# Optimization experiments

Measured on AMD Instinct MI355X. Metric: run time of the kernel, lower is better.

## Reference

```python
import jax, jax.numpy as jnp
import numpy as np

EPS_NORM = 1e-12   # F.normalize eps
EPS_Q = 1e-5       # quant scale clamp

def simple_rmsnorm(x):
    # F.normalize(x, dim=-1) * sqrt(dim)  ==  x / sqrt(mean(x^2))
    d = x.shape[-1]
    n = jnp.maximum(jnp.linalg.norm(x, axis=-1, keepdims=True), EPS_NORM)
    return x / n * jnp.sqrt(jnp.asarray(d, x.dtype))

def activation_quant(x):
    # per-token 8-bit absmax quant
    scale = 127.0 / jnp.clip(jnp.max(jnp.abs(x), axis=-1, keepdims=True), EPS_Q, None)
    return jnp.clip(jnp.round(x * scale), -128.0, 127.0) / scale

def weight_quant(w):
    # per-tensor ternary quant: scale = 1 / mean|w|
    scale = 1.0 / jnp.clip(jnp.mean(jnp.abs(w)), EPS_Q, None)
    return jnp.clip(jnp.round(w * scale), -1.0, 1.0) / scale

def bitlinear158(x, w):
    xn = simple_rmsnorm(x)
    # straight-through estimators
    xq = xn + jax.lax.stop_gradient(activation_quant(xn) - xn)
    wq = w + jax.lax.stop_gradient(weight_quant(w) - w)
    # w is [out, in] like nn.Linear
    return jnp.einsum('bsd,od->bso', xq, wq)

def setup_inputs() -> dict:
    key = jax.random.key(0)
    k1, k2, k3 = jax.random.split(key, 3)
    dim, inner = 2048, 8192
    x = jax.random.normal(k1, (4, 2048, dim), dtype=jnp.float32)
    w1 = jax.random.normal(k2, (inner, dim), dtype=jnp.float32) * 0.02
    w2 = jax.random.normal(k3, (dim, inner), dtype=jnp.float32) * 0.02
    return {"x": x, "w1": w1, "w2": w2}

def reference(x, w1, w2):
    h = bitlinear158(x, w1)
    h = jax.nn.gelu(h, approximate=False)  # nn.GELU() default = exact erf
    return bitlinear158(h, w2)
```

## Files before the change

### kernel.cpp

```cpp
#include <hip/hip_runtime.h>
#include <hip/hip_bf16.h>
#include <hip/hip_fp16.h>

typedef __attribute__((ext_vector_type(4))) int i32x4;
typedef __attribute__((ext_vector_type(8))) unsigned short u16x8;
typedef __attribute__((ext_vector_type(8))) char c8;
typedef __attribute__((ext_vector_type(4))) char c4;
typedef unsigned int u32;
typedef unsigned short u16;

#define SCH0() __builtin_amdgcn_sched_barrier(0)

__device__ __forceinline__ void gload_lds16(const void* g, void* l) {
  __builtin_amdgcn_global_load_lds((const u32 __attribute__((address_space(1)))*)g,
                                   (u32 __attribute__((address_space(3)))*)l, 16, 0, 0);
}
__device__ __forceinline__ float h2f(u16 u) { return __half2float(__ushort_as_half(u)); }
__device__ __forceinline__ u16  f2h(float f){ return __half_as_ushort(__float2half_rn(f)); }

__global__ __launch_bounds__(256) void quant_x_kernel(const float* __restrict__ x,
    char* __restrict__ qx, float* __restrict__ invs) {
  const int D = 2048;
  int row = blockIdx.x, tid = threadIdx.x;
  const float* xr = x + (size_t)row * D;
  float4 a = ((const float4*)xr)[tid * 2], b = ((const float4*)xr)[tid * 2 + 1];
  float v[8] = {a.x, a.y, a.z, a.w, b.x, b.y, b.z, b.w};
  double ss = 0; float mx = 0.0f;
#pragma unroll
  for (int i = 0; i < 8; i++) { ss += (double)v[i] * v[i]; mx = fmaxf(mx, fabsf(v[i])); }
  __shared__ double sd[256]; __shared__ float sf[256];
  sd[tid] = ss; sf[tid] = mx; __syncthreads();
  for (int o = 128; o > 0; o >>= 1) {
    if (tid < o) { sd[tid] += sd[tid + o]; sf[tid] = fmaxf(sf[tid], sf[tid + o]); }
    __syncthreads();
  }
  __shared__ float bn, bs;
  if (tid == 0) {
    float n = fmaxf((float)sqrt(sd[0]), 1e-12f);
    float amax = sf[0] * (sqrtf((float)D) / n);
    float cl = fmaxf(amax, 1e-5f);
    bn = n; bs = 127.0f / cl;
    invs[row] = cl / 127.0f;
  }
  __syncthreads();
  float n = bn, s = bs, sq = sqrtf((float)D);
  c8 q;
#pragma unroll
  for (int i = 0; i < 8; i++) {
    float xn = (v[i] / n) * sq;
    float r = rintf(xn * s);
    r = fminf(fmaxf(r, -128.0f), 127.0f);
    q[i] = (char)(int)r;
  }
  *(c8*)&qx[(size_t)row * D + tid * 8] = q;
}

__global__ __launch_bounds__(256) void absum_partial(const float* __restrict__ w,
    double* __restrict__ part, int n4) {
  int tid = threadIdx.x;
  double s = 0;
  for (int i = blockIdx.x * 256 + tid; i < n4; i += gridDim.x * 256) {
    float4 v = ((const float4*)w)[i];
    s += (double)fabsf(v.x) + (double)fabsf(v.y) + (double)fabsf(v.z) + (double)fabsf(v.w);
  }
  __shared__ double sd[256];
  sd[tid] = s; __syncthreads();
  for (int o = 128; o > 0; o >>= 1) { if (tid < o) sd[tid] += sd[tid + o]; __syncthreads(); }
  if (tid == 0) part[blockIdx.x] = sd[0];
}

__global__ __launch_bounds__(256) void wscale_final(const double* __restrict__ part,
    float* __restrict__ wsc) {
  int tid = threadIdx.x;
  __shared__ double sd[256];
  sd[tid] = part[tid] + part[tid + 256]; __syncthreads();
  for (int o = 128; o > 0; o >>= 1) { if (tid < o) sd[tid] += sd[tid + o]; __syncthreads(); }
  double s1 = sd[0]; __syncthreads();
  sd[tid] = part[512 + tid] + part[768 + tid]; __syncthreads();
  for (int o = 128; o > 0; o >>= 1) { if (tid < o) sd[tid] += sd[tid + o]; __syncthreads(); }
  if (tid == 0) {
    float m1 = (float)(s1 / 16777216.0);
    float m2 = (float)(sd[0] / 16777216.0);
    float d1 = fmaxf(m1, 1e-5f), d2 = fmaxf(m2, 1e-5f);
    wsc[0] = 1.0f / d1; wsc[1] = d1; wsc[2] = 1.0f / d2; wsc[3] = d2;
  }
}

__global__ __launch_bounds__(256) void quant_w_kernel(const float* __restrict__ w,
    char* __restrict__ q, const float* __restrict__ wsc, int widx, int n4) {
  float s = wsc[widx];
  for (int i = blockIdx.x * 256 + threadIdx.x; i < n4; i += gridDim.x * 256) {
    float4 v = ((const float4*)w)[i];
    c4 o;
    o[0] = (char)(int)(fminf(fmaxf(rintf(v.x * s), -1.0f), 1.0f));
    o[1] = (char)(int)(fminf(fmaxf(rintf(v.y * s), -1.0f), 1.0f));
    o[2] = (char)(int)(fminf(fmaxf(rintf(v.z * s), -1.0f), 1.0f));
    o[3] = (char)(int)(fminf(fmaxf(rintf(v.w * s), -1.0f), 1.0f));
    ((c4*)q)[i] = o;
  }
}

template <int EPI>
__global__ __launch_bounds__(256, 4) void gemm128(const char* __restrict__ A,
    const char* __restrict__ B, int N, int K, size_t ldA, size_t ldB, int gridN,
    const float* __restrict__ rowscale, const float* __restrict__ wsc,
    int widx, void* __restrict__ outp) {
  __shared__ __align__(16) char sm[2][2][8192];
  const int tid = threadIdx.x;
  const int lane = tid & 63, w = tid >> 6;
  const int wm = w >> 1, wn = w & 1;
  const int llo = lane & 15, lhi = lane >> 4;
  const int koff = ((lhi ^ ((llo >> 1) & 3)) << 4);

  const int nwg = gridDim.x, cpx = nwg >> 3;
  const int swz = (blockIdx.x & 7) * cpx + (blockIdx.x >> 3);
  const int bm = swz / gridN, bn = swz % gridN;

  const int NT = K >> 6;
  const size_t Abase = (size_t)(bm * 128) * ldA;
  const size_t Bbase = (size_t)(bn * 128) * ldB;

  const int r0 = tid >> 2;
  const int kb0 = (((tid & 3) ^ ((tid >> 3) & 3)) << 4);

  auto stage_tile = [&](int buf, int kt) {
    size_t ko = (size_t)kt * 64;
    gload_lds16(A + Abase + (size_t)r0 * ldA + ko + kb0,        &sm[buf][0][tid * 16]);
    gload_lds16(A + Abase + (size_t)(64 + r0) * ldA + ko + kb0, &sm[buf][0][4096 + tid * 16]);
    gload_lds16(B + Bbase + (size_t)r0 * ldB + ko + kb0,        &sm[buf][1][tid * 16]);
    gload_lds16(B + Bbase + (size_t)(64 + r0) * ldB + ko + kb0, &sm[buf][1][4096 + tid * 16]);
  };

  i32x4 a[4], b[4];
  auto readAB = [&](int buf) {
    int ra = wm * 64 + llo, rb = wn * 64 + llo;
#pragma unroll
    for (int f = 0; f < 4; f++)
      a[f] = *(const i32x4*)&sm[buf][0][(ra + f * 16) * 64 + koff];
#pragma unroll
    for (int f = 0; f < 4; f++)
      b[f] = *(const i32x4*)&sm[buf][1][(rb + f * 16) * 64 + koff];
  };

  i32x4 acc[4][4];
#pragma unroll
  for (int m = 0; m < 4; m++)
#pragma unroll
    for (int n = 0; n < 4; n++) acc[m][n] = (i32x4){0, 0, 0, 0};

  stage_tile(0, 0);
  asm volatile("s_nop 0" ::: "memory");
  stage_tile(1, 1);
  asm volatile("s_waitcnt vmcnt(4)\n\ts_barrier" ::: "memory");

  for (int t = 0; t < NT; t++) {
    const int cur = t & 1;
    readAB(cur);
    asm volatile("s_waitcnt lgkmcnt(0)\n\ts_barrier" ::: "memory");
    if (t + 2 < NT) stage_tile(cur, t + 2);
    SCH0();
    __builtin_amdgcn_s_setprio(1);
#pragma unroll
    for (int m = 0; m < 4; m++)
#pragma unroll
      for (int n = 0; n < 4; n++)
        acc[m][n] = __builtin_amdgcn_mfma_i32_16x16x64_i8(a[m], b[n], acc[m][n], 0, 0, 0);
    __builtin_amdgcn_s_setprio(0);
    if (t + 1 < NT) {
      if (t + 2 < NT) asm volatile("s_waitcnt vmcnt(4)\n\ts_barrier" ::: "memory");
      else            asm volatile("s_waitcnt vmcnt(0)\n\ts_barrier" ::: "memory");
    }
  }

  float wdeq = wsc[widx];
#pragma unroll
  for (int mf = 0; mf < 4; mf++) {
#pragma unroll
    for (int reg = 0; reg < 4; reg++) {
      int r = bm * 128 + wm * 64 + mf * 16 + lhi * 4 + reg;
      float deq = rowscale[r] * wdeq;
#pragma unroll
      for (int nf = 0; nf < 4; nf++) {
        int c = bn * 128 + wn * 64 + nf * 16 + llo;
        float val = (float)acc[mf][nf][reg] * deq;
        if (EPI == 0) {
          float g = 0.5f * val * (1.0f + erff(val * 0.70710678118654752440f));
          ((u16*)outp)[(size_t)r * N + c] = f2h(g);
        } else {
          ((float*)outp)[(size_t)r * N + c] = val;
        }
      }
    }
  }
}

__global__ __launch_bounds__(256) void quant_h_kernel(u16* __restrict__ h, float* __restrict__ invs) {
  const int D = 8192;
  int row = blockIdx.x, tid = threadIdx.x;
  u16* hr = h + (size_t)row * D;
  float v[32];
#pragma unroll
  for (int j = 0; j < 4; j++) {
    u16x8 u = *(const u16x8*)&hr[j * 2048 + tid * 8];
#pragma unroll
    for (int e = 0; e < 8; e++) v[j * 8 + e] = h2f(u[e]);
  }
  double ss = 0; float mx = 0.0f;
#pragma unroll
  for (int i = 0; i < 32; i++) { ss += (double)v[i] * v[i]; mx = fmaxf(mx, fabsf(v[i])); }
  __shared__ double sd[256]; __shared__ float sf[256];
  sd[tid] = ss; sf[tid] = mx; __syncthreads();
  for (int o = 128; o > 0; o >>= 1) {
    if (tid < o) { sd[tid] += sd[tid + o]; sf[tid] = fmaxf(sf[tid], sf[tid + o]); }
    __syncthreads();
  }
  __shared__ float bn, bs;
  if (tid == 0) {
    float n = fmaxf((float)sqrt(sd[0]), 1e-12f);
    float amax = sf[0] * (sqrtf((float)D) / n);
    float cl = fmaxf(amax, 1e-5f);
    bn = n; bs = 127.0f / cl;
    invs[row] = cl / 127.0f;
  }
  __syncthreads();
  float n = bn, s = bs, sq = sqrtf((float)D);
  char* hq = (char*)hr;
#pragma unroll
  for (int j = 0; j < 4; j++) {
    c8 q;
#pragma unroll
    for (int e = 0; e < 8; e++) {
      float xn = (v[j * 8 + e] / n) * sq;
      float r = rintf(xn * s);
      r = fminf(fmaxf(r, -128.0f), 127.0f);
      q[e] = (char)(int)r;
    }
    *(c8*)&hq[j * 2048 + tid * 8] = q;
  }
}

extern "C" void kernel_launch(void* const* d_in, const int* in_sizes, int n_in,
                              void* d_out, int out_size, void* d_ws, size_t ws_size,
                              hipStream_t stream) {
  const float* x  = (const float*)d_in[0];
  const float* w1 = (const float*)d_in[1];
  const float* w2 = (const float*)d_in[2];

  char* ws = (char*)d_ws;
  char*   qx     = (char*)(ws + 0);
  char*   w1q    = (char*)(ws + 16777216);
  char*   w2q    = (char*)(ws + 33554432);
  u16*    h      = (u16*)(ws + 50331648);
  float*  invs_x = (float*)(ws + 184549376);
  float*  invs_h = (float*)(ws + 184582144);
  double* part   = (double*)(ws + 184614912);
  float*  wsc    = (float*)(ws + 184623104);

  quant_x_kernel<<<8192, 256, 0, stream>>>(x, qx, invs_x);
  absum_partial<<<512, 256, 0, stream>>>(w1, part, 4194304);
  absum_partial<<<512, 256, 0, stream>>>(w2, part + 512, 4194304);
  wscale_final<<<1, 256, 0, stream>>>(part, wsc);
  quant_w_kernel<<<2048, 256, 0, stream>>>(w1, w1q, wsc, 0, 4194304);
  quant_w_kernel<<<2048, 256, 0, stream>>>(w2, w2q, wsc, 2, 4194304);
  gemm128<0><<<4096, 256, 0, stream>>>(qx, w1q, 8192, 2048, 2048, 2048, 64,
                                       invs_x, wsc, 1, (void*)h);
  quant_h_kernel<<<8192, 256, 0, stream>>>(h, invs_h);
  gemm128<1><<<1024, 256, 0, stream>>>((const char*)h, w2q, 2048, 8192, 16384, 8192, 16,
                                       invs_h, wsc, 3, d_out);
}
```

Before: 489.4 us.

## Load GEMM fragments directly from global memory, dropping LDS staging

Replaces the LDS double-buffered global_load_lds pipeline in the int8 GEMM with per-wave direct global loads of MFMA fragments into registers. This removes barriers, LDS traffic and the staging bookkeeping. In exchange it loses data sharing between waves (each A/B row tile is fetched by two waves) and the explicit prefetch overlap, relying on the L2/L1 caches and compiler scheduling instead.

```diff
diff --git a/kernel.cpp b/kernel.cpp
--- a/kernel.cpp
+++ b/kernel.cpp
@@ -9,12 +9,6 @@
 typedef unsigned int u32;
 typedef unsigned short u16;
 
-#define SCH0() __builtin_amdgcn_sched_barrier(0)
-
-__device__ __forceinline__ void gload_lds16(const void* g, void* l) {
-  __builtin_amdgcn_global_load_lds((const u32 __attribute__((address_space(1)))*)g,
-                                   (u32 __attribute__((address_space(3)))*)l, 16, 0, 0);
-}
 __device__ __forceinline__ float h2f(u16 u) { return __half2float(__ushort_as_half(u)); }
 __device__ __forceinline__ u16  f2h(float f){ return __half_as_ushort(__float2half_rn(f)); }
 
@@ -101,46 +95,28 @@
 }
 
 template <int EPI>
-__global__ __launch_bounds__(256, 4) void gemm128(const char* __restrict__ A,
+__global__ __launch_bounds__(256, 4) void gemm_dr(const char* __restrict__ A,
     const char* __restrict__ B, int N, int K, size_t ldA, size_t ldB, int gridN,
     const float* __restrict__ rowscale, const float* __restrict__ wsc,
     int widx, void* __restrict__ outp) {
-  __shared__ __align__(16) char sm[2][2][8192];
   const int tid = threadIdx.x;
   const int lane = tid & 63, w = tid >> 6;
   const int wm = w >> 1, wn = w & 1;
   const int llo = lane & 15, lhi = lane >> 4;
-  const int koff = ((lhi ^ ((llo >> 1) & 3)) << 4);
 
   const int nwg = gridDim.x, cpx = nwg >> 3;
   const int swz = (blockIdx.x & 7) * cpx + (blockIdx.x >> 3);
   const int bm = swz / gridN, bn = swz % gridN;
 
   const int NT = K >> 6;
-  const size_t Abase = (size_t)(bm * 128) * ldA;
-  const size_t Bbase = (size_t)(bn * 128) * ldB;
-
-  const int r0 = tid >> 2;
-  const int kb0 = (((tid & 3) ^ ((tid >> 3) & 3)) << 4);
-
-  auto stage_tile = [&](int buf, int kt) {
-    size_t ko = (size_t)kt * 64;
-    gload_lds16(A + Abase + (size_t)r0 * ldA + ko + kb0,        &sm[buf][0][tid * 16]);
-    gload_lds16(A + Abase + (size_t)(64 + r0) * ldA + ko + kb0, &sm[buf][0][4096 + tid * 16]);
-    gload_lds16(B + Bbase + (size_t)r0 * ldB + ko + kb0,        &sm[buf][1][tid * 16]);
-    gload_lds16(B + Bbase + (size_t)(64 + r0) * ldB + ko + kb0, &sm[buf][1][4096 + tid * 16]);
-  };
-
-  i32x4 a[4], b[4];
-  auto readAB = [&](int buf) {
-    int ra = wm * 64 + llo, rb = wn * 64 + llo;
-#pragma unroll
-    for (int f = 0; f < 4; f++)
-      a[f] = *(const i32x4*)&sm[buf][0][(ra + f * 16) * 64 + koff];
-#pragma unroll
-    for (int f = 0; f < 4; f++)
-      b[f] = *(const i32x4*)&sm[buf][1][(rb + f * 16) * 64 + koff];
-  };
+
+  const char* Ap[4];
+  const char* Bp[4];
+#pragma unroll
+  for (int f = 0; f < 4; f++) {
+    Ap[f] = A + (size_t)(bm * 128 + wm * 64 + f * 16 + llo) * ldA + lhi * 16;
+    Bp[f] = B + (size_t)(bn * 128 + wn * 64 + f * 16 + llo) * ldB + lhi * 16;
+  }
 
   i32x4 acc[4][4];
 #pragma unroll
@@ -148,28 +124,18 @@
 #pragma unroll
     for (int n = 0; n < 4; n++) acc[m][n] = (i32x4){0, 0, 0, 0};
 
-  stage_tile(0, 0);
-  asm volatile("s_nop 0" ::: "memory");
-  stage_tile(1, 1);
-  asm volatile("s_waitcnt vmcnt(4)\n\ts_barrier" ::: "memory");
-
   for (int t = 0; t < NT; t++) {
-    const int cur = t & 1;
-    readAB(cur);
-    asm volatile("s_waitcnt lgkmcnt(0)\n\ts_barrier" ::: "memory");
-    if (t + 2 < NT) stage_tile(cur, t + 2);
-    SCH0();
-    __builtin_amdgcn_s_setprio(1);
+    const size_t ko = (size_t)t * 64;
+    i32x4 a[4], b[4];
+#pragma unroll
+    for (int f = 0; f < 4; f++) a[f] = *(const i32x4*)(Ap[f] + ko);
+#pragma unroll
+    for (int f = 0; f < 4; f++) b[f] = *(const i32x4*)(Bp[f] + ko);
 #pragma unroll
     for (int m = 0; m < 4; m++)
 #pragma unroll
       for (int n = 0; n < 4; n++)
         acc[m][n] = __builtin_amdgcn_mfma_i32_16x16x64_i8(a[m], b[n], acc[m][n], 0, 0, 0);
-    __builtin_amdgcn_s_setprio(0);
-    if (t + 1 < NT) {
-      if (t + 2 < NT) asm volatile("s_waitcnt vmcnt(4)\n\ts_barrier" ::: "memory");
-      else            asm volatile("s_waitcnt vmcnt(0)\n\ts_barrier" ::: "memory");
-    }
   }
 
   float wdeq = wsc[widx];
@@ -262,9 +228,9 @@
   wscale_final<<<1, 256, 0, stream>>>(part, wsc);
   quant_w_kernel<<<2048, 256, 0, stream>>>(w1, w1q, wsc, 0, 4194304);
   quant_w_kernel<<<2048, 256, 0, stream>>>(w2, w2q, wsc, 2, 4194304);
-  gemm128<0><<<4096, 256, 0, stream>>>(qx, w1q, 8192, 2048, 2048, 2048, 64,
+  gemm_dr<0><<<4096, 256, 0, stream>>>(qx, w1q, 8192, 2048, 2048, 2048, 64,
                                        invs_x, wsc, 1, (void*)h);
   quant_h_kernel<<<8192, 256, 0, stream>>>(h, invs_h);
-  gemm128<1><<<1024, 256, 0, stream>>>((const char*)h, w2q, 2048, 8192, 16384, 8192, 16,
+  gemm_dr<1><<<1024, 256, 0, stream>>>((const char*)h, w2q, 2048, 8192, 16384, 8192, 16,
                                        invs_h, wsc, 3, d_out);
 }
```

New measurement: 1.076 ms. +119.9%, slower.
